# Kernel optimization log

Hardware: AMD Instinct MI355X
Metric: run time of the kernel (lower is better)

Reference implementation:

```python
import jax, jax.numpy as jnp
import numpy as np

B, T, C, H = 2, 2048, 2048, 16  # batch, seq_len, dim, num_heads
D = C // H  # head_dim = 128
ROPE_BASE = 10000.0


def apply_rope(x, pos):
    # x: [B, T, H, D]; adjacent-pair rotation (torchtune convention)
    d = x.shape[-1]
    inv_freq = 1.0 / (ROPE_BASE ** (jnp.arange(0, d, 2, dtype=jnp.float32) / d))  # [D/2]
    freqs = pos.astype(jnp.float32)[:, None] * inv_freq[None, :]                 # [T, D/2]
    cos = jnp.cos(freqs)[None, :, None, :]
    sin = jnp.sin(freqs)[None, :, None, :]
    x1 = x[..., 0::2]
    x2 = x[..., 1::2]
    out = jnp.stack([x1 * cos - x2 * sin, x2 * cos + x1 * sin], axis=-1)  # [B,T,H,D/2,2]
    return out.reshape(x.shape)


def setup_inputs() -> dict:
    key = jax.random.key(0)
    k1, k2, k3 = jax.random.split(key, 3)
    x = jax.random.normal(k1, (B, T, C), dtype=jnp.float32)
    # 0.02 init scale keeps attention logits in a sane range
    W_qkv = jax.random.normal(k2, (C, 3 * C), dtype=jnp.float32) * 0.02
    W_out = jax.random.normal(k3, (C, C), dtype=jnp.float32) * 0.02
    return {"x": x, "W_qkv": W_qkv, "W_out": W_out}


def reference(x, W_qkv, W_out):
    b, t, c = x.shape
    h, d = H, c // H
    # fused QKV projection
    qkv = (x @ W_qkv).reshape(b, t, 3, h, d)
    q, k, v = qkv[:, :, 0], qkv[:, :, 1], qkv[:, :, 2]  # [B,T,H,D] each
    pos = jnp.arange(t)  # cache_pos = 0 (prefill)
    q = apply_rope(q, pos)
    k = apply_rope(k, pos)
    scale = 1.0 / np.sqrt(d).astype(np.float32)
    scores = jnp.einsum('bqhd,bkhd->bhqk', q, k) * scale  # [B,H,T,T]
    causal = jnp.tril(jnp.ones((t, t), dtype=bool))
    scores = jnp.where(causal[None, None], scores, -jnp.inf)
    probs = jax.nn.softmax(scores, axis=-1)
    o = jnp.einsum('bhqk,bkhd->bqhd', probs, v).reshape(b, t, c)
    return o @ W_out
```

## Files before the change

kernel.cpp:

```cpp
#include <hip/hip_runtime.h>
#include <stdint.h>

#define TSEQ 2048

typedef __bf16 bf16x8 __attribute__((ext_vector_type(8)));
typedef float f32x4 __attribute__((ext_vector_type(4)));

typedef const __attribute__((address_space(1))) unsigned int* gas_u32;
typedef __attribute__((address_space(3))) unsigned int* las_u32;

__device__ __forceinline__ f32x4 mfma16(bf16x8 a, bf16x8 b, f32x4 c) {
  return __builtin_amdgcn_mfma_f32_16x16x32_bf16(a, b, c, 0, 0, 0);
}

__device__ __forceinline__ unsigned short f2b(float f) {
  unsigned int u = __float_as_uint(f);
  u += 0x7fffu + ((u >> 16) & 1u);
  return (unsigned short)(u >> 16);
}

__device__ __forceinline__ void gload_lds16(const unsigned short* g, unsigned short* l) {
  __builtin_amdgcn_global_load_lds((gas_u32)(const void*)g, (las_u32)(void*)l, 16, 0, 0);
}

__global__ __launch_bounds__(256) void cast_bf16_kernel(const float* __restrict__ src,
                                                        unsigned short* __restrict__ dst) {
  size_t i = ((size_t)blockIdx.x * 256 + threadIdx.x) * 4;
  float4 v = *(const float4*)(src + i);
  ushort4 o;
  o.x = f2b(v.x); o.y = f2b(v.y); o.z = f2b(v.z); o.w = f2b(v.w);
  *(ushort4*)(dst + i) = o;
}

__global__ __launch_bounds__(256) void transpose_cast_kernel(const float* __restrict__ src,
                                                             unsigned short* __restrict__ dst,
                                                             int R, int Cc) {
  __shared__ float tile[64][65];
  int cb = blockIdx.x * 64;
  int rb = blockIdx.y * 64;
  int t = threadIdx.x;
  int tr = t >> 4;
  int tc = (t & 15) * 4;
#pragma unroll
  for (int i = 0; i < 4; i++) {
    int r = tr + 16 * i;
    float4 v = *(const float4*)(src + (size_t)(rb + r) * Cc + cb + tc);
    tile[r][tc + 0] = v.x; tile[r][tc + 1] = v.y;
    tile[r][tc + 2] = v.z; tile[r][tc + 3] = v.w;
  }
  __syncthreads();
#pragma unroll
  for (int i = 0; i < 4; i++) {
    int r2 = tr + 16 * i;
    ushort4 o;
    o.x = f2b(tile[tc + 0][r2]);
    o.y = f2b(tile[tc + 1][r2]);
    o.z = f2b(tile[tc + 2][r2]);
    o.w = f2b(tile[tc + 3][r2]);
    *(ushort4*)(dst + (size_t)(cb + r2) * R + rb + tc) = o;
  }
}

__device__ __forceinline__ void gemm_core_256(const unsigned short* __restrict__ A,
                                              const unsigned short* __restrict__ Bt,
                                              int K, int bm, int bn,
                                              unsigned short* sm,
                                              f32x4 (&acc)[4][4]) {
  const int t = threadIdx.x;
  const int lane = t & 63, w = t >> 6;
  const int wm = (w >> 2) * 64;
  const int wn = (w & 3) * 64;
  const int quad = lane >> 4, l16 = lane & 15;
  const int rsw = l16 & 7;

  const int srow = t >> 3;
  const int gch = (t & 7) ^ (srow & 7);
  const unsigned short* pA = A + (size_t)(bm + srow) * K + gch * 8;
  const unsigned short* pB = Bt + (size_t)(bn + srow) * K + gch * 8;
  const size_t K64 = (size_t)64 * K;

  auto stageA = [&](int k0, unsigned short* dstSlot) {
    gload_lds16(pA + k0, dstSlot + t * 8);
    gload_lds16(pA + K64 + k0, dstSlot + (t + 512) * 8);
  };
  auto stageB01 = [&](int k0, unsigned short* dstSlot) {
    unsigned short* tB = dstSlot + 8192;
    gload_lds16(pB + k0, tB + t * 8);
    gload_lds16(pB + K64 + k0, tB + (t + 512) * 8);
  };
  auto stageB23 = [&](int k0, unsigned short* dstSlot) {
    unsigned short* tB = dstSlot + 8192;
    gload_lds16(pB + 2 * K64 + k0, tB + (t + 1024) * 8);
    gload_lds16(pB + 3 * K64 + k0, tB + (t + 1536) * 8);
  };

  stageA(0, sm);          stageB01(0, sm);          stageB23(0, sm);
  stageA(64, sm + 24576); stageB01(64, sm + 24576); stageB23(64, sm + 24576);

  const int nIter = K >> 6;
  int scur = 0, sstg = 2;

#pragma unroll 1
  for (int it = 0; it < nIter; it++) {
    if (it + 1 < nIter)
      asm volatile("s_waitcnt vmcnt(6) lgkmcnt(0)" ::: "memory");
    else
      asm volatile("s_waitcnt vmcnt(0) lgkmcnt(0)" ::: "memory");
    __builtin_amdgcn_s_barrier();
    asm volatile("" ::: "memory");

    const unsigned short* sA = sm + scur * 24576;
    const unsigned short* sB = sA + 8192;
    unsigned short* tgt = sm + sstg * 24576;
    const bool doStage = (it + 2 < nIter);
    const int k2 = (it + 2) << 6;

    bf16x8 aF[2][2], b0[2][2], b1[2][2];

    auto mm8 = [&](int ib, int jb, bf16x8 (&af)[2][2], bf16x8 (&bf)[2][2]) {
      __builtin_amdgcn_s_setprio(1);
#pragma unroll
      for (int i2 = 0; i2 < 2; i2++)
#pragma unroll
        for (int j2 = 0; j2 < 2; j2++)
#pragma unroll
          for (int kk = 0; kk < 2; kk++)
            acc[ib + i2][jb + j2] = mfma16(af[i2][kk], bf[j2][kk], acc[ib + i2][jb + j2]);
      __builtin_amdgcn_s_setprio(0);
    };

#pragma unroll
    for (int i2 = 0; i2 < 2; i2++)
#pragma unroll
      for (int kk = 0; kk < 2; kk++)
        aF[i2][kk] = *(const bf16x8*)(sA + (wm + i2 * 16 + l16) * 64 + (((kk * 4 + quad) ^ rsw) * 8));
#pragma unroll
    for (int j2 = 0; j2 < 2; j2++)
#pragma unroll
      for (int kk = 0; kk < 2; kk++)
        b0[j2][kk] = *(const bf16x8*)(sB + (wn + j2 * 16 + l16) * 64 + (((kk * 4 + quad) ^ rsw) * 8));
    if (doStage) stageA(k2, tgt);
    mm8(0, 0, aF, b0);

#pragma unroll
    for (int j2 = 0; j2 < 2; j2++)
#pragma unroll
      for (int kk = 0; kk < 2; kk++)
        b1[j2][kk] = *(const bf16x8*)(sB + (wn + (2 + j2) * 16 + l16) * 64 + (((kk * 4 + quad) ^ rsw) * 8));
    if (doStage) stageB01(k2, tgt);
    mm8(0, 2, aF, b1);

#pragma unroll
    for (int i2 = 0; i2 < 2; i2++)
#pragma unroll
      for (int kk = 0; kk < 2; kk++)
        aF[i2][kk] = *(const bf16x8*)(sA + (wm + (2 + i2) * 16 + l16) * 64 + (((kk * 4 + quad) ^ rsw) * 8));
    if (doStage) stageB23(k2, tgt);
    mm8(2, 2, aF, b1);

    mm8(2, 0, aF, b0);

    scur = (scur == 2) ? 0 : scur + 1;
    sstg = (sstg == 2) ? 0 : sstg + 1;
  }
  __syncthreads();
}

__global__ __launch_bounds__(512, 2) void gemm_qkv_rope(const unsigned short* __restrict__ Xb,
                                                        const unsigned short* __restrict__ Wqt,
                                                        unsigned short* __restrict__ Qd,
                                                        unsigned short* __restrict__ Kd,
                                                        unsigned short* __restrict__ Vtd) {
  __shared__ unsigned short smem[73728];
  f32x4 acc[4][4];
  const f32x4 z = {0.f, 0.f, 0.f, 0.f};
#pragma unroll
  for (int i = 0; i < 4; i++)
#pragma unroll
    for (int j = 0; j < 4; j++) acc[i][j] = z;

  const int bm = blockIdx.y * 128;
  const int bn = blockIdx.x * 256;
  gemm_core_256(Xb, Wqt, 2048, bm, bn, smem, acc);

  const int c0 = blockIdx.x * 2;
  const int s = c0 >> 4;
  const int hA = c0 & 15, hB = (c0 + 1) & 15;
  const int t = threadIdx.x, lane = t & 63, w = t >> 6;
  const int wm = (w >> 2) * 64, wn = (w & 3) * 64;
  const int quad = lane >> 4, l16 = lane & 15;
  const int bq = bm >> 11;
  const int tpos0 = bm & (TSEQ - 1);
  unsigned short* sC = smem;

  if (s < 2) {
    const float scl = (s == 0) ? 0.08838834764831845f : 1.0f;
#pragma unroll
    for (int j = 0; j < 4; j++) {
      int d = wn + j * 16 + l16;
      int dh = d & 127;
      float invf = __expf(-(float)(dh >> 1) * 0.14391157f);
#pragma unroll
      for (int i = 0; i < 4; i++) {
#pragma unroll
        for (int r = 0; r < 4; r++) {
          int row = wm + i * 16 + quad * 4 + r;
          float ang = (float)(tpos0 + row) * invf;
          float sn, cs;
          __sincosf(ang, &sn, &cs);
          float v = acc[i][j][r];
          float p = __shfl_xor(v, 1, 64);
          float outv = (d & 1) ? (v * cs + p * sn) : (v * cs - p * sn);
          sC[row * 264 + d] = f2b(outv * scl);
        }
      }
    }
    __syncthreads();
    unsigned short* dst = (s == 0) ? Qd : Kd;
#pragma unroll
    for (int it = 0; it < 8; it++) {
      int u = t + 512 * it;
      int row = u >> 5, cc = u & 31;
      int hl = cc >> 4;
      size_t gb = ((size_t)(bq * 16 + (hl ? hB : hA)) * TSEQ + tpos0 + row) * 128 + (cc & 15) * 8;
      *(uint4*)(dst + gb) = *(const uint4*)(sC + row * 264 + cc * 8);
    }
  } else {
#pragma unroll
    for (int j = 0; j < 4; j++) {
      int d = wn + j * 16 + l16;
#pragma unroll
      for (int i = 0; i < 4; i++)
#pragma unroll
        for (int r = 0; r < 4; r++) {
          int col = wm + i * 16 + quad * 4 + r;
          sC[d * 136 + col] = f2b(acc[i][j][r]);
        }
    }
    __syncthreads();
#pragma unroll
    for (int it = 0; it < 8; it++) {
      int u = t + 512 * it;
      int dd = u >> 4, cc = u & 15;
      int hl = dd >> 7, dl = dd & 127;
      size_t gb = ((size_t)(bq * 16 + (hl ? hB : hA)) * 128 + dl) * TSEQ + tpos0 + cc * 8;
      *(uint4*)(Vtd + gb) = *(const uint4*)(sC + dd * 136 + cc * 8);
    }
  }
}

__global__ __launch_bounds__(256, 2) void attn_kernel(const unsigned short* __restrict__ Q,
                                                      const unsigned short* __restrict__ Kmat,
                                                      const unsigned short* __restrict__ Vt,
                                                      unsigned short* __restrict__ Ob) {
  __shared__ unsigned short smem[37376];
  const int pair = blockIdx.x, bh = blockIdx.y;
  const int qA = pair, qB = 31 - pair;
  const int t = threadIdx.x, lane = t & 63, w = t >> 6, quad = lane >> 4, l16 = lane & 15;
  const size_t base = (size_t)bh * TSEQ * 128;
  const unsigned short* Qp = Q + base;
  const unsigned short* Kp = Kmat + base;
  const unsigned short* Vp = Vt + base;
  unsigned short* myP = smem + 32768 + w * 1152;

  bf16x8 aqA[4], aqB[4];
  {
    int qrA = qA * 64 + w * 16 + l16;
    int qrB = qB * 64 + w * 16 + l16;
#pragma unroll
    for (int kk = 0; kk < 4; kk++) {
      aqA[kk] = *(const bf16x8*)(Qp + (size_t)qrA * 128 + kk * 32 + quad * 8);
      aqB[kk] = *(const bf16x8*)(Qp + (size_t)qrB * 128 + kk * 32 + quad * 8);
    }
  }
  const f32x4 z = {0.f, 0.f, 0.f, 0.f};
  f32x4 oA[8], oB[8];
  float mA[4], lA[4], mB[4], lB[4];
#pragma unroll
  for (int dt = 0; dt < 8; dt++) { oA[dt] = z; oB[dt] = z; }
#pragma unroll
  for (int r = 0; r < 4; r++) { mA[r] = -1e30f; lA[r] = 0.f; mB[r] = -1e30f; lB[r] = 0.f; }

  auto load_tiles = [&](int kb, int buf) {
    unsigned short* bK = smem + buf * 16384;
    unsigned short* bV = bK + 8192;
    const unsigned short* Kt = Kp + (size_t)kb * 64 * 128;
#pragma unroll
    for (int i2 = 0; i2 < 4; i2++) {
      int idx = t + 256 * i2;
      int r = idx >> 4, cS = idx & 15;
      int c = cS ^ (r & 7);
      gload_lds16(Kt + r * 128 + c * 8, bK + idx * 8);
    }
#pragma unroll
    for (int i2 = 0; i2 < 4; i2++) {
      int idx = t + 256 * i2;
      int r = idx >> 3, cS = idx & 7;
      int c = cS ^ (r & 7);
      gload_lds16(Vp + (size_t)r * TSEQ + kb * 64 + c * 8, bV + idx * 8);
    }
  };

  auto process = [&](bf16x8 (&aq)[4], f32x4 (&o)[8], float (&mst)[4], float (&lst)[4],
                     int qb, int kb, const unsigned short* bK, const unsigned short* bV) {
    f32x4 S[4];
#pragma unroll
    for (int nt = 0; nt < 4; nt++) {
      f32x4 sacc = z;
#pragma unroll
      for (int kk = 0; kk < 4; kk++) {
        const unsigned short* p =
            bK + (nt * 16 + l16) * 128 + (((kk * 4 + quad) ^ (l16 & 7)) * 8);
        sacc = mfma16(aq[kk], *(const bf16x8*)p, sacc);
      }
      S[nt] = sacc;
    }
    if (kb == qb) {
      int qg = qb * 64 + w * 16 + quad * 4;
#pragma unroll
      for (int nt = 0; nt < 4; nt++) {
        int key = kb * 64 + nt * 16 + l16;
#pragma unroll
        for (int r = 0; r < 4; r++)
          if (key > qg + r) S[nt][r] = -1e30f;
      }
    }
    float alpha[4];
#pragma unroll
    for (int r = 0; r < 4; r++) {
      float mx = fmaxf(fmaxf(S[0][r], S[1][r]), fmaxf(S[2][r], S[3][r]));
      mx = fmaxf(mx, __shfl_xor(mx, 1, 64));
      mx = fmaxf(mx, __shfl_xor(mx, 2, 64));
      mx = fmaxf(mx, __shfl_xor(mx, 4, 64));
      mx = fmaxf(mx, __shfl_xor(mx, 8, 64));
      float mnew = fmaxf(mst[r], mx);
      alpha[r] = __expf(mst[r] - mnew);
      mst[r] = mnew;
    }
    float rs[4] = {0.f, 0.f, 0.f, 0.f};
#pragma unroll
    for (int nt = 0; nt < 4; nt++)
#pragma unroll
      for (int r = 0; r < 4; r++) {
        float p = __expf(S[nt][r] - mst[r]);
        S[nt][r] = p;
        rs[r] += p;
      }
#pragma unroll
    for (int r = 0; r < 4; r++) {
      float s4 = rs[r];
      s4 += __shfl_xor(s4, 1, 64);
      s4 += __shfl_xor(s4, 2, 64);
      s4 += __shfl_xor(s4, 4, 64);
      s4 += __shfl_xor(s4, 8, 64);
      lst[r] = lst[r] * alpha[r] + s4;
#pragma unroll
      for (int nt = 0; nt < 4; nt++)
        myP[(quad * 4 + r) * 72 + nt * 16 + l16] = f2b(S[nt][r]);
    }
#pragma unroll
    for (int dt = 0; dt < 8; dt++) {
      f32x4 ov = o[dt];
      ov[0] *= alpha[0]; ov[1] *= alpha[1]; ov[2] *= alpha[2]; ov[3] *= alpha[3];
      o[dt] = ov;
    }
#pragma unroll
    for (int kk = 0; kk < 2; kk++) {
      bf16x8 ap = *(const bf16x8*)(myP + l16 * 72 + kk * 32 + quad * 8);
#pragma unroll
      for (int dt = 0; dt < 8; dt++) {
        const unsigned short* p =
            bV + (dt * 16 + l16) * 64 + (((kk * 4 + quad) ^ (l16 & 7)) * 8);
        o[dt] = mfma16(ap, *(const bf16x8*)p, o[dt]);
      }
    }
  };

  load_tiles(0, 0);
#pragma unroll 1
  for (int kb = 0; kb <= qB; kb++) {
    __syncthreads();
    if (kb < qB) load_tiles(kb + 1, (kb + 1) & 1);
    const unsigned short* bK = smem + (kb & 1) * 16384;
    const unsigned short* bV = bK + 8192;
    process(aqB, oB, mB, lB, qB, kb, bK, bV);
    if (kb <= qA) process(aqA, oA, mA, lA, qA, kb, bK, bV);
  }

  __syncthreads();
  unsigned short* sOA = smem;
  unsigned short* sOB = smem + 8704;
#pragma unroll
  for (int dt = 0; dt < 8; dt++)
#pragma unroll
    for (int r = 0; r < 4; r++) {
      int row = w * 16 + quad * 4 + r;
      sOA[row * 136 + dt * 16 + l16] = f2b(oA[dt][r] / lA[r]);
      sOB[row * 136 + dt * 16 + l16] = f2b(oB[dt][r] / lB[r]);
    }
  __syncthreads();
  const int b = bh >> 4, h = bh & 15;
#pragma unroll
  for (int it = 0; it < 4; it++) {
    int c = t + 256 * it;
    int row = c >> 4, off = (c & 15) * 8;
    uint4 va = *(const uint4*)(sOA + row * 136 + off);
    *(uint4*)(Ob + (size_t)(b * TSEQ + qA * 64 + row) * 2048 + h * 128 + off) = va;
    uint4 vb = *(const uint4*)(sOB + row * 136 + off);
    *(uint4*)(Ob + (size_t)(b * TSEQ + qB * 64 + row) * 2048 + h * 128 + off) = vb;
  }
}

__global__ __launch_bounds__(512, 2) void gemm_out_kernel(const unsigned short* __restrict__ Ob,
                                                          const unsigned short* __restrict__ Wot,
                                                          float* __restrict__ Cout) {
  __shared__ unsigned short smem[73728];
  f32x4 acc[4][4];
  const f32x4 z = {0.f, 0.f, 0.f, 0.f};
#pragma unroll
  for (int i = 0; i < 4; i++)
#pragma unroll
    for (int j = 0; j < 4; j++) acc[i][j] = z;

  const int bm = blockIdx.y * 128, bn = blockIdx.x * 256;
  gemm_core_256(Ob, Wot, 2048, bm, bn, smem, acc);

  const int t = threadIdx.x, lane = t & 63, w = t >> 6;
  const int wm = (w >> 2) * 64, wn = (w & 3) * 64;
  const int quad = lane >> 4, l16 = lane & 15;
#pragma unroll
  for (int i = 0; i < 4; i++)
#pragma unroll
    for (int j = 0; j < 4; j++)
#pragma unroll
      for (int r = 0; r < 4; r++) {
        int row = bm + wm + i * 16 + quad * 4 + r;
        int col = bn + wn + j * 16 + l16;
        Cout[(size_t)row * 2048 + col] = acc[i][j][r];
      }
}

extern "C" void kernel_launch(void* const* d_in, const int* in_sizes, int n_in,
                              void* d_out, int out_size, void* d_ws, size_t ws_size,
                              hipStream_t stream) {
  (void)in_sizes; (void)n_in; (void)out_size; (void)ws_size;
  const float* x = (const float*)d_in[0];
  const float* Wqkv = (const float*)d_in[1];
  const float* Wout = (const float*)d_in[2];
  float* out = (float*)d_out;
  char* ws = (char*)d_ws;

  unsigned short* Xb  = (unsigned short*)(ws);
  unsigned short* Wqt = (unsigned short*)(ws + 16777216);
  unsigned short* Wot = (unsigned short*)(ws + 41943040);
  unsigned short* Qd  = (unsigned short*)(ws + 50331648);
  unsigned short* Kd  = (unsigned short*)(ws + 67108864);
  unsigned short* Vtd = (unsigned short*)(ws + 83886080);
  unsigned short* Obf = (unsigned short*)(ws + 100663296);

  cast_bf16_kernel<<<8192, 256, 0, stream>>>(x, Xb);
  transpose_cast_kernel<<<dim3(96, 32), 256, 0, stream>>>(Wqkv, Wqt, 2048, 6144);
  transpose_cast_kernel<<<dim3(32, 32), 256, 0, stream>>>(Wout, Wot, 2048, 2048);
  gemm_qkv_rope<<<dim3(24, 32), 512, 0, stream>>>(Xb, Wqt, Qd, Kd, Vtd);
  attn_kernel<<<dim3(16, 32), 256, 0, stream>>>(Qd, Kd, Vtd, Obf);
  gemm_out_kernel<<<dim3(8, 32), 512, 0, stream>>>(Obf, Wot, out);
}
```

Measured before the change: 374.5 us.

## Split GEMM K-dimension across wave groups with larger per-wave tiles and LDS reduction

The 8 waves of each GEMM block are regrouped as 4 spatial tiles of 64x128, with the two wave halves each handling one 32-wide K half of every 64-wide K step. Each wave now loads 4 A and 8 B fragments per step and issues 32 MFMAs, which raises operand reuse per LDS read. At the end, the two K halves exchange and sum partial accumulators through LDS, and the epilogues are remapped so each wave writes the 32 rows it kept. This doubles accumulator registers per wave, 128 floats, which under launch_bounds(512,2) may cause spilling, and it adds a reduction pass plus an extra barrier.

New measurement: 552.4 us. 47.5% more time.

```diff
diff --git a/kernel.cpp b/kernel.cpp
--- a/kernel.cpp
+++ b/kernel.cpp
@@ -65,13 +65,16 @@
                                               const unsigned short* __restrict__ Bt,
                                               int K, int bm, int bn,
                                               unsigned short* sm,
-                                              f32x4 (&acc)[4][4]) {
+                                              f32x4 (&acc)[4][8]) {
   const int t = threadIdx.x;
   const int lane = t & 63, w = t >> 6;
-  const int wm = (w >> 2) * 64;
-  const int wn = (w & 3) * 64;
+  const int wloc = w & 3;
+  const int wm = (wloc >> 1) * 64;
+  const int wn = (wloc & 1) * 128;
+  const int ks = w >> 2;
   const int quad = lane >> 4, l16 = lane & 15;
   const int rsw = l16 & 7;
+  const int ch = ((ks * 4 + quad) ^ rsw) * 8;
 
   const int srow = t >> 3;
   const int gch = (t & 7) ^ (srow & 7);
@@ -115,55 +118,66 @@
     const bool doStage = (it + 2 < nIter);
     const int k2 = (it + 2) << 6;
 
-    bf16x8 aF[2][2], b0[2][2], b1[2][2];
-
-    auto mm8 = [&](int ib, int jb, bf16x8 (&af)[2][2], bf16x8 (&bf)[2][2]) {
+    bf16x8 aF[4], bF[8];
+
+    auto mm = [&](int jb) {
       __builtin_amdgcn_s_setprio(1);
 #pragma unroll
-      for (int i2 = 0; i2 < 2; i2++)
+      for (int i = 0; i < 4; i++)
 #pragma unroll
         for (int j2 = 0; j2 < 2; j2++)
-#pragma unroll
-          for (int kk = 0; kk < 2; kk++)
-            acc[ib + i2][jb + j2] = mfma16(af[i2][kk], bf[j2][kk], acc[ib + i2][jb + j2]);
+          acc[i][jb + j2] = mfma16(aF[i], bF[jb + j2], acc[i][jb + j2]);
       __builtin_amdgcn_s_setprio(0);
     };
 
 #pragma unroll
-    for (int i2 = 0; i2 < 2; i2++)
-#pragma unroll
-      for (int kk = 0; kk < 2; kk++)
-        aF[i2][kk] = *(const bf16x8*)(sA + (wm + i2 * 16 + l16) * 64 + (((kk * 4 + quad) ^ rsw) * 8));
-#pragma unroll
-    for (int j2 = 0; j2 < 2; j2++)
-#pragma unroll
-      for (int kk = 0; kk < 2; kk++)
-        b0[j2][kk] = *(const bf16x8*)(sB + (wn + j2 * 16 + l16) * 64 + (((kk * 4 + quad) ^ rsw) * 8));
+    for (int i = 0; i < 4; i++)
+      aF[i] = *(const bf16x8*)(sA + (wm + i * 16 + l16) * 64 + ch);
+#pragma unroll
+    for (int j = 0; j < 2; j++)
+      bF[j] = *(const bf16x8*)(sB + (wn + j * 16 + l16) * 64 + ch);
     if (doStage) stageA(k2, tgt);
-    mm8(0, 0, aF, b0);
-
-#pragma unroll
-    for (int j2 = 0; j2 < 2; j2++)
-#pragma unroll
-      for (int kk = 0; kk < 2; kk++)
-        b1[j2][kk] = *(const bf16x8*)(sB + (wn + (2 + j2) * 16 + l16) * 64 + (((kk * 4 + quad) ^ rsw) * 8));
+    mm(0);
+#pragma unroll
+    for (int j = 2; j < 4; j++)
+      bF[j] = *(const bf16x8*)(sB + (wn + j * 16 + l16) * 64 + ch);
     if (doStage) stageB01(k2, tgt);
-    mm8(0, 2, aF, b1);
-
-#pragma unroll
-    for (int i2 = 0; i2 < 2; i2++)
-#pragma unroll
-      for (int kk = 0; kk < 2; kk++)
-        aF[i2][kk] = *(const bf16x8*)(sA + (wm + (2 + i2) * 16 + l16) * 64 + (((kk * 4 + quad) ^ rsw) * 8));
+    mm(2);
+#pragma unroll
+    for (int j = 4; j < 6; j++)
+      bF[j] = *(const bf16x8*)(sB + (wn + j * 16 + l16) * 64 + ch);
     if (doStage) stageB23(k2, tgt);
-    mm8(2, 2, aF, b1);
-
-    mm8(2, 0, aF, b0);
+    mm(4);
+#pragma unroll
+    for (int j = 6; j < 8; j++)
+      bF[j] = *(const bf16x8*)(sB + (wn + j * 16 + l16) * 64 + ch);
+    mm(6);
 
     scur = (scur == 2) ? 0 : scur + 1;
     sstg = (sstg == 2) ? 0 : sstg + 1;
   }
   __syncthreads();
+
+  {
+    float* mbuf = (float*)sm;
+    const int give0 = (w < 4) ? 2 : 0;
+    const int keep0 = 2 - give0;
+    float* wb = mbuf + w * 4096;
+#pragma unroll
+    for (int i2 = 0; i2 < 2; i2++)
+#pragma unroll
+      for (int j = 0; j < 8; j++)
+        *(f32x4*)(wb + (i2 * 8 + j) * 256 + lane * 4) = acc[give0 + i2][j];
+    __syncthreads();
+    const float* pb = mbuf + (w ^ 4) * 4096;
+#pragma unroll
+    for (int i2 = 0; i2 < 2; i2++)
+#pragma unroll
+      for (int j = 0; j < 8; j++) {
+        f32x4 v = *(const f32x4*)(pb + (i2 * 8 + j) * 256 + lane * 4);
+        acc[keep0 + i2][j] += v;
+      }
+  }
 }
 
 __global__ __launch_bounds__(512, 2) void gemm_qkv_rope(const unsigned short* __restrict__ Xb,
@@ -172,12 +186,12 @@
                                                         unsigned short* __restrict__ Kd,
                                                         unsigned short* __restrict__ Vtd) {
   __shared__ unsigned short smem[73728];
-  f32x4 acc[4][4];
+  f32x4 acc[4][8];
   const f32x4 z = {0.f, 0.f, 0.f, 0.f};
 #pragma unroll
   for (int i = 0; i < 4; i++)
 #pragma unroll
-    for (int j = 0; j < 4; j++) acc[i][j] = z;
+    for (int j = 0; j < 8; j++) acc[i][j] = z;
 
   const int bm = blockIdx.y * 128;
   const int bn = blockIdx.x * 256;
@@ -187,28 +201,33 @@
   const int s = c0 >> 4;
   const int hA = c0 & 15, hB = (c0 + 1) & 15;
   const int t = threadIdx.x, lane = t & 63, w = t >> 6;
-  const int wm = (w >> 2) * 64, wn = (w & 3) * 64;
+  const int wloc = w & 3;
+  const int wm = (wloc >> 1) * 64, wn = (wloc & 1) * 128;
+  const int keep0 = (w < 4) ? 0 : 2;
+  const int rowbase = wm + (w >> 2) * 32;
   const int quad = lane >> 4, l16 = lane & 15;
   const int bq = bm >> 11;
   const int tpos0 = bm & (TSEQ - 1);
+
+  __syncthreads();
   unsigned short* sC = smem;
 
   if (s < 2) {
     const float scl = (s == 0) ? 0.08838834764831845f : 1.0f;
 #pragma unroll
-    for (int j = 0; j < 4; j++) {
+    for (int j = 0; j < 8; j++) {
       int d = wn + j * 16 + l16;
       int dh = d & 127;
       float invf = __expf(-(float)(dh >> 1) * 0.14391157f);
 #pragma unroll
-      for (int i = 0; i < 4; i++) {
+      for (int i = 0; i < 2; i++) {
 #pragma unroll
         for (int r = 0; r < 4; r++) {
-          int row = wm + i * 16 + quad * 4 + r;
+          int row = rowbase + i * 16 + quad * 4 + r;
           float ang = (float)(tpos0 + row) * invf;
           float sn, cs;
           __sincosf(ang, &sn, &cs);
-          float v = acc[i][j][r];
+          float v = acc[keep0 + i][j][r];
           float p = __shfl_xor(v, 1, 64);
           float outv = (d & 1) ? (v * cs + p * sn) : (v * cs - p * sn);
           sC[row * 264 + d] = f2b(outv * scl);
@@ -227,14 +246,14 @@
     }
   } else {
 #pragma unroll
-    for (int j = 0; j < 4; j++) {
+    for (int j = 0; j < 8; j++) {
       int d = wn + j * 16 + l16;
 #pragma unroll
-      for (int i = 0; i < 4; i++)
+      for (int i = 0; i < 2; i++)
 #pragma unroll
         for (int r = 0; r < 4; r++) {
-          int col = wm + i * 16 + quad * 4 + r;
-          sC[d * 136 + col] = f2b(acc[i][j][r]);
+          int col = rowbase + i * 16 + quad * 4 + r;
+          sC[d * 136 + col] = f2b(acc[keep0 + i][j][r]);
         }
     }
     __syncthreads();
@@ -415,28 +434,31 @@
                                                           const unsigned short* __restrict__ Wot,
                                                           float* __restrict__ Cout) {
   __shared__ unsigned short smem[73728];
-  f32x4 acc[4][4];
+  f32x4 acc[4][8];
   const f32x4 z = {0.f, 0.f, 0.f, 0.f};
 #pragma unroll
   for (int i = 0; i < 4; i++)
 #pragma unroll
-    for (int j = 0; j < 4; j++) acc[i][j] = z;
+    for (int j = 0; j < 8; j++) acc[i][j] = z;
 
   const int bm = blockIdx.y * 128, bn = blockIdx.x * 256;
   gemm_core_256(Ob, Wot, 2048, bm, bn, smem, acc);
 
   const int t = threadIdx.x, lane = t & 63, w = t >> 6;
-  const int wm = (w >> 2) * 64, wn = (w & 3) * 64;
+  const int wloc = w & 3;
+  const int wm = (wloc >> 1) * 64, wn = (wloc & 1) * 128;
+  const int keep0 = (w < 4) ? 0 : 2;
+  const int rowbase = wm + (w >> 2) * 32;
   const int quad = lane >> 4, l16 = lane & 15;
 #pragma unroll
-  for (int i = 0; i < 4; i++)
-#pragma unroll
-    for (int j = 0; j < 4; j++)
+  for (int i = 0; i < 2; i++)
+#pragma unroll
+    for (int j = 0; j < 8; j++)
 #pragma unroll
       for (int r = 0; r < 4; r++) {
-        int row = bm + wm + i * 16 + quad * 4 + r;
+        int row = bm + rowbase + i * 16 + quad * 4 + r;
         int col = bn + wn + j * 16 + l16;
-        Cout[(size_t)row * 2048 + col] = acc[i][j][r];
+        Cout[(size_t)row * 2048 + col] = acc[keep0 + i][j][r];
       }
 }
 
```
